# Kernel tuning notes

Measured on AMD Instinct MI355X. Metric: run time of the kernel, lower is better.

The kernel has to match this reference:

```python
import jax, jax.numpy as jnp
import numpy as np

B, S, D = 4, 8192, 512      # batch, seq_len, dim
P, M = 32, 2048             # num_persistent_memory, memory_size
EPS = 1e-5


def setup_inputs() -> dict:
    key = jax.random.key(0)
    ks = jax.random.split(key, 8)
    s = 1.0 / np.sqrt(D)

    def lin_w(k):
        return jax.random.uniform(k, (D, D), jnp.float32, -s, s)

    return {
        "x": jax.random.normal(ks[0], (B, S, D), jnp.float32),
        "persistent_memory": jax.random.normal(ks[1], (P, D), jnp.float32),
        "Wk": lin_w(ks[2]), "bk": jnp.zeros((D,), jnp.float32),
        "Wv": lin_w(ks[3]), "bv": jnp.zeros((D,), jnp.float32),
        "Wq": lin_w(ks[4]), "bq": jnp.zeros((D,), jnp.float32),
        "gamma": jnp.ones((D,), jnp.float32),
        "beta": jnp.zeros((D,), jnp.float32),
        "Wout": lin_w(ks[5]), "bout": jnp.zeros((D,), jnp.float32),
    }


def reference(x, persistent_memory, Wk, bk, Wv, bv, Wq, bq, gamma, beta, Wout, bout):
    b = x.shape[0]
    # concat persistent tokens: [B, T, D], T = P + S
    pm = jnp.broadcast_to(persistent_memory[None], (b, P, D))
    c = jnp.concatenate([pm, x], axis=1)

    k = c @ Wk + bk
    v = c @ Wv + bv
    q = c @ Wq + bq
    scale = 1.0 / jnp.sqrt(jnp.asarray(D, c.dtype))

    # init_state -> zeros [B, M, D]
    state0 = jnp.zeros((b, M, D), c.dtype)

    # update: write combined tokens into memory slots via cross-attention
    write_attn = jax.nn.softmax(jnp.einsum('bmd,btd->bmt', state0, k) * scale, axis=-1)  # [B,M,T]
    state = state0 + jnp.einsum('bmt,btd->bmd', write_attn, v)                           # [B,M,D]

    # retrieve: read memory with projected queries
    read_attn = jax.nn.softmax(jnp.einsum('btd,bmd->btm', q, state) * scale, axis=-1)    # [B,T,M]
    mem_out = jnp.einsum('btm,bmd->btd', read_attn, state)                               # [B,T,D]

    # LayerNorm
    mu = jnp.mean(mem_out, axis=-1, keepdims=True)
    var = jnp.mean((mem_out - mu) ** 2, axis=-1, keepdims=True)
    normed = (mem_out - mu) / jnp.sqrt(var + EPS) * gamma + beta

    # output projection (dropout is identity in eval mode)
    return normed @ Wout + bout
```

## Files before the change

### kernel.cpp

```cpp
#include <hip/hip_runtime.h>
#include <math.h>

#define BB 4
#define SS 8192
#define DD 512
#define PP 32
#define TT (PP + SS)
#define EPSV 1e-5f


__global__ __launch_bounds__(512) void k_colsum(const float4* __restrict__ x4,
                                                float* __restrict__ csum) {
  const int bb    = blockIdx.x >> 7;
  const int chunk = blockIdx.x & 127;
  const int tid   = threadIdx.x;

  const float4* p = x4 + ((size_t)bb * SS + (size_t)chunk * 64) * (DD / 4);

  float ax = 0.f, ay = 0.f, az = 0.f, aw = 0.f;
#pragma unroll
  for (int i = 0; i < 16; ++i) {
    float4 t = p[i * 512 + tid];
    ax += t.x; ay += t.y; az += t.z; aw += t.w;
  }

  __shared__ float4 sh[512];
  sh[tid] = make_float4(ax, ay, az, aw);
  __syncthreads();

  if (tid < 128) {
    float4 a0 = sh[tid], a1 = sh[tid + 128], a2 = sh[tid + 256], a3 = sh[tid + 384];
    float* dst = csum + bb * DD + tid * 4;
    atomicAdd(dst + 0, a0.x + a1.x + a2.x + a3.x);
    atomicAdd(dst + 1, a0.y + a1.y + a2.y + a3.y);
    atomicAdd(dst + 2, a0.z + a1.z + a2.z + a3.z);
    atomicAdd(dst + 3, a0.w + a1.w + a2.w + a3.w);
  }
}

__global__ __launch_bounds__(512) void k_vbar(const float* __restrict__ csum,
                                              const float* __restrict__ pm,
                                              const float* __restrict__ Wv,
                                              float* __restrict__ vbar) {
  const int bb = blockIdx.x >> 5;
  const int ch = blockIdx.x & 31;
  const int j  = threadIdx.x;

  __shared__ float a[16];
  if (j < 16) {
    const int d = ch * 16 + j;
    float s = csum[bb * DD + d];
#pragma unroll
    for (int p = 0; p < PP; ++p) s += pm[p * DD + d];
    a[j] = s * (1.0f / (float)TT);
  }
  __syncthreads();

  float acc = 0.f;
#pragma unroll
  for (int i = 0; i < 16; ++i)
    acc += a[i] * Wv[(ch * 16 + i) * DD + j];

  atomicAdd(&vbar[bb * DD + j], acc);
}

__global__ __launch_bounds__(512) void k_zmat(const float* __restrict__ vbar,
                                              const float* __restrict__ bv,
                                              const float* __restrict__ gamma,
                                              const float* __restrict__ beta,
                                              const float* __restrict__ Wout,
                                              float* __restrict__ z) {
  const int bb = blockIdx.x >> 5;
  const int ch = blockIdx.x & 31;
  const int j  = threadIdx.x;

  const float v = vbar[bb * DD + j] + bv[j];

  float v1 = v, v2 = v * v;
#pragma unroll
  for (int off = 32; off > 0; off >>= 1) {
    v1 += __shfl_down(v1, off, 64);
    v2 += __shfl_down(v2, off, 64);
  }
  __shared__ float w1[8], w2[8];
  const int wave = j >> 6;
  if ((j & 63) == 0) { w1[wave] = v1; w2[wave] = v2; }
  __syncthreads();
  float t1 = 0.f, t2 = 0.f;
#pragma unroll
  for (int w = 0; w < 8; ++w) { t1 += w1[w]; t2 += w2[w]; }
  const float mu  = t1 * (1.0f / (float)DD);
  const float var = t2 * (1.0f / (float)DD) - mu * mu;
  const float inv = 1.0f / sqrtf(var + EPSV);

  __shared__ float y[DD];
  y[j] = (v - mu) * inv * gamma[j] + beta[j];
  __syncthreads();

  float acc = 0.f;
#pragma unroll
  for (int i = 0; i < 16; ++i)
    acc += y[ch * 16 + i] * Wout[(ch * 16 + i) * DD + j];

  atomicAdd(&z[bb * DD + j], acc);
}

__global__ __launch_bounds__(256) void k_bcast(const float4* __restrict__ z4,
                                               const float4* __restrict__ bout4,
                                               float4* __restrict__ out4) {
  const unsigned i  = blockIdx.x * 256u + threadIdx.x;
  const unsigned bb = i / 1052672u;
  const unsigned j4 = i & 127u;
  float4 zz = z4[bb * 128u + j4];
  float4 bo = bout4[j4];
  out4[i] = make_float4(zz.x + bo.x, zz.y + bo.y, zz.z + bo.z, zz.w + bo.w);
}

extern "C" void kernel_launch(void* const* d_in, const int* in_sizes, int n_in,
                              void* d_out, int out_size, void* d_ws, size_t ws_size,
                              hipStream_t stream) {
  const float* x     = (const float*)d_in[0];
  const float* pm    = (const float*)d_in[1];
  const float* Wv    = (const float*)d_in[4];
  const float* bv    = (const float*)d_in[5];
  const float* gamma = (const float*)d_in[8];
  const float* beta  = (const float*)d_in[9];
  const float* Wout  = (const float*)d_in[10];
  const float* bout  = (const float*)d_in[11];

  float* csum = (float*)d_ws;
  float* vbar = csum + BB * DD;
  float* z    = vbar + BB * DD;

  hipMemsetAsync(csum, 0, 3 * BB * DD * sizeof(float), stream);

  k_colsum<<<BB * 128, 512, 0, stream>>>((const float4*)x, csum);

  k_vbar<<<BB * 32, 512, 0, stream>>>(csum, pm, Wv, vbar);

  k_zmat<<<BB * 32, 512, 0, stream>>>(vbar, bv, gamma, beta, Wout, z);

  const unsigned total4 = (unsigned)BB * TT * DD / 4;
  k_bcast<<<total4 / 256, 256, 0, stream>>>((const float4*)z,
                                            (const float4*)bout,
                                            (float4*)d_out);
}
```

Baseline: 153.9 us.

## Fuse four stages into one persistent kernel with global barriers

```diff
diff --git a/kernel.cpp b/kernel.cpp
--- a/kernel.cpp
+++ b/kernel.cpp
@@ -7,113 +7,141 @@
 #define PP 32
 #define TT (PP + SS)
 #define EPSV 1e-5f
+#define NB 512
 
 
-__global__ __launch_bounds__(512) void k_colsum(const float4* __restrict__ x4,
-                                                float* __restrict__ csum) {
-  const int bb    = blockIdx.x >> 7;
-  const int chunk = blockIdx.x & 127;
-  const int tid   = threadIdx.x;
+#define LOAD_A(p)    __hip_atomic_load((p), __ATOMIC_RELAXED, __HIP_MEMORY_SCOPE_AGENT)
+#define STORE_A(p,v) __hip_atomic_store((p), (v), __ATOMIC_RELAXED, __HIP_MEMORY_SCOPE_AGENT)
 
-  const float4* p = x4 + ((size_t)bb * SS + (size_t)chunk * 64) * (DD / 4);
-
-  float ax = 0.f, ay = 0.f, az = 0.f, aw = 0.f;
-#pragma unroll
-  for (int i = 0; i < 16; ++i) {
-    float4 t = p[i * 512 + tid];
-    ax += t.x; ay += t.y; az += t.z; aw += t.w;
+__device__ __forceinline__ void gbar(unsigned* cnt, unsigned target) {
+  __syncthreads();
+  if (threadIdx.x == 0) {
+    __threadfence();
+    __hip_atomic_fetch_add(cnt, 1u, __ATOMIC_ACQ_REL, __HIP_MEMORY_SCOPE_AGENT);
+    while (__hip_atomic_load(cnt, __ATOMIC_ACQUIRE, __HIP_MEMORY_SCOPE_AGENT) < target)
+      __builtin_amdgcn_s_sleep(1);
+    __threadfence();
   }
-
-  __shared__ float4 sh[512];
-  sh[tid] = make_float4(ax, ay, az, aw);
   __syncthreads();
-
-  if (tid < 128) {
-    float4 a0 = sh[tid], a1 = sh[tid + 128], a2 = sh[tid + 256], a3 = sh[tid + 384];
-    float* dst = csum + bb * DD + tid * 4;
-    atomicAdd(dst + 0, a0.x + a1.x + a2.x + a3.x);
-    atomicAdd(dst + 1, a0.y + a1.y + a2.y + a3.y);
-    atomicAdd(dst + 2, a0.z + a1.z + a2.z + a3.z);
-    atomicAdd(dst + 3, a0.w + a1.w + a2.w + a3.w);
-  }
 }
 
-__global__ __launch_bounds__(512) void k_vbar(const float* __restrict__ csum,
-                                              const float* __restrict__ pm,
-                                              const float* __restrict__ Wv,
-                                              float* __restrict__ vbar) {
-  const int bb = blockIdx.x >> 5;
-  const int ch = blockIdx.x & 31;
-  const int j  = threadIdx.x;
+__global__ __launch_bounds__(512, 4) void k_fused(
+    const float4* __restrict__ x4, const float* __restrict__ pm,
+    const float* __restrict__ Wv, const float* __restrict__ bv,
+    const float* __restrict__ gamma, const float* __restrict__ beta,
+    const float* __restrict__ Wout, const float* __restrict__ bout,
+    float* __restrict__ ws, float4* __restrict__ out4) {
+  unsigned* cnt   = (unsigned*)ws;
+  float*    part  = ws + 4;
+  float*    vpart = part + NB * DD;
+  float*    zpart = vpart + 128 * DD;
 
-  __shared__ float a[16];
-  if (j < 16) {
-    const int d = ch * 16 + j;
-    float s = csum[bb * DD + d];
+  const int tid = threadIdx.x;
+  const int blk = blockIdx.x;
+
+  __shared__ float4 sh4[512];
+  __shared__ float  aSh[16];
+  __shared__ float  ySh[DD];
+  __shared__ float  w1[8], w2[8];
+  __shared__ float  zSh[BB * DD];
+
+  {
+    const int bb    = blk >> 7;
+    const int chunk = blk & 127;
+    const float4* p = x4 + ((size_t)bb * SS + (size_t)chunk * 64) * (DD / 4);
+    float ax = 0.f, ay = 0.f, az = 0.f, aw = 0.f;
 #pragma unroll
-    for (int p = 0; p < PP; ++p) s += pm[p * DD + d];
-    a[j] = s * (1.0f / (float)TT);
+    for (int i = 0; i < 16; ++i) {
+      float4 t = p[i * 512 + tid];
+      ax += t.x; ay += t.y; az += t.z; aw += t.w;
+    }
+    sh4[tid] = make_float4(ax, ay, az, aw);
+    __syncthreads();
+    if (tid < 128) {
+      float4 a0 = sh4[tid], a1 = sh4[tid + 128], a2 = sh4[tid + 256], a3 = sh4[tid + 384];
+      float* dst = part + blk * DD + tid * 4;
+      STORE_A(dst + 0, a0.x + a1.x + a2.x + a3.x);
+      STORE_A(dst + 1, a0.y + a1.y + a2.y + a3.y);
+      STORE_A(dst + 2, a0.z + a1.z + a2.z + a3.z);
+      STORE_A(dst + 3, a0.w + a1.w + a2.w + a3.w);
+    }
   }
-  __syncthreads();
+  gbar(cnt, NB);
 
-  float acc = 0.f;
+  if (blk < 128) {
+    const int bb  = blk >> 5;
+    const int ch  = blk & 31;
+    const int d16 = tid >> 5;
+    const int lane = tid & 31;
+    const int col = ch * 16 + d16;
+    float s = 0.f;
 #pragma unroll
-  for (int i = 0; i < 16; ++i)
-    acc += a[i] * Wv[(ch * 16 + i) * DD + j];
+    for (int k = 0; k < 4; ++k)
+      s += LOAD_A(&part[(size_t)(bb * 128 + lane + 32 * k) * DD + col]);
+    s += pm[lane * DD + col];
+#pragma unroll
+    for (int off = 16; off > 0; off >>= 1) s += __shfl_down(s, off, 32);
+    if (lane == 0) aSh[d16] = s * (1.0f / (float)TT);
+    __syncthreads();
+    float acc = 0.f;
+#pragma unroll
+    for (int i = 0; i < 16; ++i)
+      acc += aSh[i] * Wv[(ch * 16 + i) * DD + tid];
+    STORE_A(&vpart[(bb * 32 + ch) * DD + tid], acc);
+  }
+  gbar(cnt, 2 * NB);
 
-  atomicAdd(&vbar[bb * DD + j], acc);
-}
+  if (blk < 128) {
+    const int bb = blk >> 5;
+    const int ch = blk & 31;
+    float v = bv[tid];
+#pragma unroll
+    for (int c = 0; c < 32; ++c) v += LOAD_A(&vpart[(bb * 32 + c) * DD + tid]);
 
-__global__ __launch_bounds__(512) void k_zmat(const float* __restrict__ vbar,
-                                              const float* __restrict__ bv,
-                                              const float* __restrict__ gamma,
-                                              const float* __restrict__ beta,
-                                              const float* __restrict__ Wout,
-                                              float* __restrict__ z) {
-  const int bb = blockIdx.x >> 5;
-  const int ch = blockIdx.x & 31;
-  const int j  = threadIdx.x;
+    float v1 = v, v2 = v * v;
+#pragma unroll
+    for (int off = 32; off > 0; off >>= 1) {
+      v1 += __shfl_down(v1, off, 64);
+      v2 += __shfl_down(v2, off, 64);
+    }
+    const int wave = tid >> 6;
+    if ((tid & 63) == 0) { w1[wave] = v1; w2[wave] = v2; }
+    __syncthreads();
+    float t1 = 0.f, t2 = 0.f;
+#pragma unroll
+    for (int w = 0; w < 8; ++w) { t1 += w1[w]; t2 += w2[w]; }
+    const float mu  = t1 * (1.0f / (float)DD);
+    const float var = t2 * (1.0f / (float)DD) - mu * mu;
+    const float inv = 1.0f / sqrtf(var + EPSV);
+    ySh[tid] = (v - mu) * inv * gamma[tid] + beta[tid];
+    __syncthreads();
 
-  const float v = vbar[bb * DD + j] + bv[j];
+    float acc = 0.f;
+#pragma unroll
+    for (int i = 0; i < 16; ++i)
+      acc += ySh[ch * 16 + i] * Wout[(ch * 16 + i) * DD + tid];
+    STORE_A(&zpart[(bb * 32 + ch) * DD + tid], acc);
+  }
+  gbar(cnt, 3 * NB);
 
-  float v1 = v, v2 = v * v;
+  {
 #pragma unroll
-  for (int off = 32; off > 0; off >>= 1) {
-    v1 += __shfl_down(v1, off, 64);
-    v2 += __shfl_down(v2, off, 64);
+    for (int bb = 0; bb < BB; ++bb) {
+      float acc = bout[tid];
+#pragma unroll 8
+      for (int c = 0; c < 32; ++c)
+        acc += LOAD_A(&zpart[(bb * 32 + c) * DD + tid]);
+      zSh[bb * DD + tid] = acc;
+    }
+    __syncthreads();
+    const float4* z4 = (const float4*)zSh;
+    const unsigned total4 = (unsigned)BB * TT * DD / 4;
+    for (unsigned i = blk * 512u + tid; i < total4; i += NB * 512u) {
+      const unsigned bb = i / 1052672u;
+      const unsigned j4 = i & 127u;
+      out4[i] = z4[bb * 128u + j4];
+    }
   }
-  __shared__ float w1[8], w2[8];
-  const int wave = j >> 6;
-  if ((j & 63) == 0) { w1[wave] = v1; w2[wave] = v2; }
-  __syncthreads();
-  float t1 = 0.f, t2 = 0.f;
-#pragma unroll
-  for (int w = 0; w < 8; ++w) { t1 += w1[w]; t2 += w2[w]; }
-  const float mu  = t1 * (1.0f / (float)DD);
-  const float var = t2 * (1.0f / (float)DD) - mu * mu;
-  const float inv = 1.0f / sqrtf(var + EPSV);
-
-  __shared__ float y[DD];
-  y[j] = (v - mu) * inv * gamma[j] + beta[j];
-  __syncthreads();
-
-  float acc = 0.f;
-#pragma unroll
-  for (int i = 0; i < 16; ++i)
-    acc += y[ch * 16 + i] * Wout[(ch * 16 + i) * DD + j];
-
-  atomicAdd(&z[bb * DD + j], acc);
-}
-
-__global__ __launch_bounds__(256) void k_bcast(const float4* __restrict__ z4,
-                                               const float4* __restrict__ bout4,
-                                               float4* __restrict__ out4) {
-  const unsigned i  = blockIdx.x * 256u + threadIdx.x;
-  const unsigned bb = i / 1052672u;
-  const unsigned j4 = i & 127u;
-  float4 zz = z4[bb * 128u + j4];
-  float4 bo = bout4[j4];
-  out4[i] = make_float4(zz.x + bo.x, zz.y + bo.y, zz.z + bo.z, zz.w + bo.w);
 }
 
 extern "C" void kernel_launch(void* const* d_in, const int* in_sizes, int n_in,
@@ -128,20 +156,8 @@
   const float* Wout  = (const float*)d_in[10];
   const float* bout  = (const float*)d_in[11];
 
-  float* csum = (float*)d_ws;
-  float* vbar = csum + BB * DD;
-  float* z    = vbar + BB * DD;
+  hipMemsetAsync(d_ws, 0, 16, stream);
 
-  hipMemsetAsync(csum, 0, 3 * BB * DD * sizeof(float), stream);
-
-  k_colsum<<<BB * 128, 512, 0, stream>>>((const float4*)x, csum);
-
-  k_vbar<<<BB * 32, 512, 0, stream>>>(csum, pm, Wv, vbar);
-
-  k_zmat<<<BB * 32, 512, 0, stream>>>(vbar, bv, gamma, beta, Wout, z);
-
-  const unsigned total4 = (unsigned)BB * TT * DD / 4;
-  k_bcast<<<total4 / 256, 256, 0, stream>>>((const float4*)z,
-                                            (const float4*)bout,
-                                            (float4*)d_out);
+  k_fused<<<NB, 512, 0, stream>>>((const float4*)x, pm, Wv, bv, gamma, beta,
+                                  Wout, bout, (float*)d_ws, (float4*)d_out);
 }
```

New measurement: 377.2 us. +145.1%, slower.

## Replace atomic column sums with partial buffers and drop the memset

Applied to the files above, without the earlier changes.

```diff
diff --git a/kernel.cpp b/kernel.cpp
--- a/kernel.cpp
+++ b/kernel.cpp
@@ -10,16 +10,16 @@
 
 
 __global__ __launch_bounds__(512) void k_colsum(const float4* __restrict__ x4,
-                                                float* __restrict__ csum) {
-  const int bb    = blockIdx.x >> 7;
-  const int chunk = blockIdx.x & 127;
+                                                float4* __restrict__ part4) {
+  const int bb    = blockIdx.x >> 8;
+  const int chunk = blockIdx.x & 255;
   const int tid   = threadIdx.x;
 
-  const float4* p = x4 + ((size_t)bb * SS + (size_t)chunk * 64) * (DD / 4);
+  const float4* p = x4 + ((size_t)bb * SS + (size_t)chunk * 32) * (DD / 4);
 
   float ax = 0.f, ay = 0.f, az = 0.f, aw = 0.f;
 #pragma unroll
-  for (int i = 0; i < 16; ++i) {
+  for (int i = 0; i < 8; ++i) {
     float4 t = p[i * 512 + tid];
     ax += t.x; ay += t.y; az += t.z; aw += t.w;
   }
@@ -30,41 +30,47 @@
 
   if (tid < 128) {
     float4 a0 = sh[tid], a1 = sh[tid + 128], a2 = sh[tid + 256], a3 = sh[tid + 384];
-    float* dst = csum + bb * DD + tid * 4;
-    atomicAdd(dst + 0, a0.x + a1.x + a2.x + a3.x);
-    atomicAdd(dst + 1, a0.y + a1.y + a2.y + a3.y);
-    atomicAdd(dst + 2, a0.z + a1.z + a2.z + a3.z);
-    atomicAdd(dst + 3, a0.w + a1.w + a2.w + a3.w);
+    part4[blockIdx.x * 128 + tid] =
+        make_float4(a0.x + a1.x + a2.x + a3.x, a0.y + a1.y + a2.y + a3.y,
+                    a0.z + a1.z + a2.z + a3.z, a0.w + a1.w + a2.w + a3.w);
   }
 }
 
-__global__ __launch_bounds__(512) void k_vbar(const float* __restrict__ csum,
+__global__ __launch_bounds__(512) void k_vbar(const float* __restrict__ part,
                                               const float* __restrict__ pm,
                                               const float* __restrict__ Wv,
-                                              float* __restrict__ vbar) {
+                                              float* __restrict__ vpart,
+                                              float* __restrict__ z) {
   const int bb = blockIdx.x >> 5;
   const int ch = blockIdx.x & 31;
   const int j  = threadIdx.x;
 
-  __shared__ float a[16];
-  if (j < 16) {
-    const int d = ch * 16 + j;
-    float s = csum[bb * DD + d];
+  __shared__ float aSh[16];
+  {
+    const int d16  = j >> 5;
+    const int lane = j & 31;
+    const int col  = ch * 16 + d16;
+    float s = 0.f;
 #pragma unroll
-    for (int p = 0; p < PP; ++p) s += pm[p * DD + d];
-    a[j] = s * (1.0f / (float)TT);
+    for (int k = 0; k < 8; ++k)
+      s += part[(size_t)(bb * 256 + lane + 32 * k) * DD + col];
+    s += pm[lane * DD + col];
+#pragma unroll
+    for (int off = 16; off > 0; off >>= 1) s += __shfl_down(s, off, 32);
+    if (lane == 0) aSh[d16] = s * (1.0f / (float)TT);
   }
   __syncthreads();
 
   float acc = 0.f;
 #pragma unroll
   for (int i = 0; i < 16; ++i)
-    acc += a[i] * Wv[(ch * 16 + i) * DD + j];
+    acc += aSh[i] * Wv[(ch * 16 + i) * DD + j];
+  vpart[(bb * 32 + ch) * DD + j] = acc;
 
-  atomicAdd(&vbar[bb * DD + j], acc);
+  if (blockIdx.x < BB) z[blockIdx.x * DD + j] = 0.f;
 }
 
-__global__ __launch_bounds__(512) void k_zmat(const float* __restrict__ vbar,
+__global__ __launch_bounds__(512) void k_zmat(const float* __restrict__ vpart,
                                               const float* __restrict__ bv,
                                               const float* __restrict__ gamma,
                                               const float* __restrict__ beta,
@@ -74,7 +80,9 @@
   const int ch = blockIdx.x & 31;
   const int j  = threadIdx.x;
 
-  const float v = vbar[bb * DD + j] + bv[j];
+  float v = bv[j];
+#pragma unroll
+  for (int c = 0; c < 32; ++c) v += vpart[(bb * 32 + c) * DD + j];
 
   float v1 = v, v2 = v * v;
 #pragma unroll
@@ -101,7 +109,6 @@
 #pragma unroll
   for (int i = 0; i < 16; ++i)
     acc += y[ch * 16 + i] * Wout[(ch * 16 + i) * DD + j];
-
   atomicAdd(&z[bb * DD + j], acc);
 }
 
@@ -128,17 +135,15 @@
   const float* Wout  = (const float*)d_in[10];
   const float* bout  = (const float*)d_in[11];
 
-  float* csum = (float*)d_ws;
-  float* vbar = csum + BB * DD;
-  float* z    = vbar + BB * DD;
+  float* part  = (float*)d_ws;
+  float* vpart = part + 1024 * DD;
+  float* z     = vpart + 128 * DD;
 
-  hipMemsetAsync(csum, 0, 3 * BB * DD * sizeof(float), stream);
+  k_colsum<<<1024, 512, 0, stream>>>((const float4*)x, (float4*)part);
 
-  k_colsum<<<BB * 128, 512, 0, stream>>>((const float4*)x, csum);
+  k_vbar<<<BB * 32, 512, 0, stream>>>(part, pm, Wv, vpart, z);
 
-  k_vbar<<<BB * 32, 512, 0, stream>>>(csum, pm, Wv, vbar);
-
-  k_zmat<<<BB * 32, 512, 0, stream>>>(vbar, bv, gamma, beta, Wout, z);
+  k_zmat<<<BB * 32, 512, 0, stream>>>(vpart, bv, gamma, beta, Wout, z);
 
   const unsigned total4 = (unsigned)BB * TT * DD / 4;
   k_bcast<<<total4 / 256, 256, 0, stream>>>((const float4*)z,
```

Result: faster. 141.9 us (-7.8%).
